# Optimization experiments

Measured on AMD Instinct MI355X. Metric: run time of the kernel, lower is better.

## Reference

```python
import jax, jax.numpy as jnp
import numpy as np

U = 256  # units


def _lstm_scan(x, W, R, bc):
    """Run the custom LSTM over time axis of x [B,T,D].

    W: (D,4U) stacked [ki|kf|ko|kc]; R: (U,4U) stacked [ri|rf|ro|rc]; bc: (U,).
    Faithful quirks: no bias on i/f/o gates; c_new = sigmoid(f*c + i*cand);
    h_new = tanh(c_new) * o.
    Returns (last_h [B,U], outputs [B,T,U]).
    """
    B = x.shape[0]
    xW = jnp.einsum('btd,dg->tbg', x, W)  # precompute input projections, (T,B,4U)

    def step(carry, xw):
        h, c = carry
        g = xw + h @ R  # (B,4U)
        i = jax.nn.sigmoid(g[:, 0 * U:1 * U])
        f = jax.nn.sigmoid(g[:, 1 * U:2 * U])
        o = jax.nn.sigmoid(g[:, 2 * U:3 * U])
        cand = jnp.tanh(g[:, 3 * U:4 * U] + bc)
        c_new = jax.nn.sigmoid(f * c + i * cand)
        h_new = jnp.tanh(c_new) * o
        return (h_new, c_new), h_new

    h0 = jnp.zeros((B, U), dtype=x.dtype)
    c0 = jnp.zeros((B, U), dtype=x.dtype)
    (h_last, _), hs = jax.lax.scan(step, (h0, c0), xW)
    return h_last, jnp.swapaxes(hs, 0, 1)  # (B,T,U)


def setup_inputs() -> dict:
    key = jax.random.key(0)
    ks = jax.random.split(key, 5)
    B, T, D = 16, 2048, 256
    s_in = 1.0 / np.sqrt(D)
    s_rec = 1.0 / np.sqrt(U)
    return {
        'x': jax.random.normal(ks[0], (B, T, D), dtype=jnp.float32),
        'W_f': jax.random.normal(ks[1], (D, 4 * U), dtype=jnp.float32) * s_in,
        'R_f': jax.random.normal(ks[2], (U, 4 * U), dtype=jnp.float32) * s_rec,
        'bc_f': jnp.zeros((U,), dtype=jnp.float32),
        'W_b': jax.random.normal(ks[3], (D, 4 * U), dtype=jnp.float32) * s_in,
        'R_b': jax.random.normal(ks[4], (U, 4 * U), dtype=jnp.float32) * s_rec,
        'bc_b': jnp.zeros((U,), dtype=jnp.float32),
    }


def reference(x, W_f, R_f, bc_f, W_b, R_b, bc_b):
    # forward direction
    _, out_f = _lstm_scan(x, W_f, R_f, bc_f)
    # backward direction: K.rnn(go_backwards=True) iterates reversed inputs and
    # returns outputs in iteration (reversed-time) order, NOT re-reversed.
    _, out_b = _lstm_scan(x[:, ::-1, :], W_b, R_b, bc_b)
    return jnp.concatenate([out_f, out_b], axis=-1)  # (B,T,2U)
```

## Files before the change

kernel.cpp:

```cpp
#include <hip/hip_runtime.h>
#include <hip/hip_bf16.h>
#include <hip/hip_fp16.h>

#define TT 2048
#define BB 16
#define DD 256
#define GG 1024
#define UU 256

using f32x4  = __attribute__((ext_vector_type(4))) float;
using short8 = __attribute__((ext_vector_type(8))) short;
using f16x8  = __attribute__((ext_vector_type(8))) _Float16;
using u32x4  = __attribute__((ext_vector_type(4))) unsigned int;

static __device__ __forceinline__ unsigned short f2h_u(float f){
  _Float16 h = (_Float16)f;
  return __builtin_bit_cast(unsigned short, h);
}
static __device__ __forceinline__ float h2f(unsigned short u){
  return (float)__builtin_bit_cast(_Float16, u);
}
static __device__ __forceinline__ unsigned short f2bf_u(float f){
  __hip_bfloat16 b = __float2bfloat16(f);
  return __builtin_bit_cast(unsigned short, b);
}
static __device__ __forceinline__ float sigmoid_f(float x){
  return 1.0f / (1.0f + __expf(-x));
}
static __device__ __forceinline__ float tanh_f(float x){
  float ax = fabsf(x);
  float e  = __expf(2.0f*ax);
  float r  = 1.0f - 2.0f/(e + 1.0f);
  return copysignf(r, x);
}
static __device__ __forceinline__ f32x4 mfma16x16x32_f16(f16x8 a, f16x8 b, f32x4 c){
  return __builtin_amdgcn_mfma_f32_16x16x32_f16(a, b, c, 0, 0, 0);
}
static __device__ __forceinline__ void lds_barrier(){
  __builtin_amdgcn_sched_barrier(0);
  asm volatile("s_waitcnt lgkmcnt(0)" ::: "memory");
  __builtin_amdgcn_s_barrier();
  __builtin_amdgcn_sched_barrier(0);
}

__global__ __launch_bounds__(256) void cvt_x_kernel(const float* __restrict__ x,
                                                    unsigned short* __restrict__ xh){
  int gid = blockIdx.x*256 + threadIdx.x;
  const float4* xv = (const float4*)x;
  float4 v = xv[gid];
  unsigned int u0 = (unsigned int)f2bf_u(v.x) | ((unsigned int)f2bf_u(v.y) << 16);
  unsigned int u1 = (unsigned int)f2bf_u(v.z) | ((unsigned int)f2bf_u(v.w) << 16);
  ((uint2*)xh)[gid] = make_uint2(u0, u1);
}

__global__ __launch_bounds__(256) void cvt_wt_kernel(const float* __restrict__ Wf,
                                                     const float* __restrict__ Wb,
                                                     unsigned short* __restrict__ wt){
  int gid = blockIdx.x*256 + threadIdx.x;
  int d   = gid >> 18;
  int rem = gid & 262143;
  int n   = rem >> 8;
  int k   = rem & 255;
  const float* src = d ? Wb : Wf;
  wt[gid] = f2bf_u(src[k*GG + n]);
}

__global__ __launch_bounds__(256) void cvt_rt_kernel(const float* __restrict__ Rf,
                                                     const float* __restrict__ Rb,
                                                     unsigned short* __restrict__ rt){
  int gid = blockIdx.x*256 + threadIdx.x;
  int d   = gid >> 18;
  int rem = gid & 262143;
  int c   = rem >> 8;
  int p   = rem & 255;
  int Qb  = c >> 7, tc = c & 127;
  int ul  = tc >> 2, g = tc & 3;
  int ucol = g*256 + Qb*32 + ul;
  int s = p >> 5, l4g = (p >> 3) & 3, e = p & 7;
  int k = 32*s + (e < 4 ? 4*l4g + e : 16 + 4*l4g + (e - 4));
  const float* src = d ? Rb : Rf;
  rt[gid] = f2h_u(src[k*GG + ucol]);
}

__global__ __launch_bounds__(256) void gemm_projT(const unsigned short* __restrict__ Ah,
                                                  const unsigned short* __restrict__ BTh,
                                                  unsigned short* __restrict__ Cd,
                                                  int xstart, int Tc){
  __shared__ __align__(16) unsigned short smem[18432];
  unsigned short* sA = smem;
  unsigned short* sB = smem + 9216;
  unsigned short* sC = smem;

  int mt  = blockIdx.x >> 3;
  int nt  = blockIdx.x & 7;
  int tid = threadIdx.x;

  const unsigned short* Bb = BTh + (size_t)nt*128*DD;

  int w = tid >> 6, lane = tid & 63, l15 = lane & 15, l4 = lane >> 4;
  int wm = w >> 1, wn = w & 1;

  f32x4 zero4 = {0.0f, 0.0f, 0.0f, 0.0f};
  f32x4 acc[4][4];
#pragma unroll
  for (int i = 0; i < 4; ++i)
#pragma unroll
    for (int j = 0; j < 4; ++j) acc[i][j] = zero4;

  for (int kt = 0; kt < 4; ++kt){
    __syncthreads();
#pragma unroll
    for (int i = 0; i < 4; ++i){
      int ch = tid + i*256;
      int r = ch >> 3, c8 = ch & 7;
      int bb = r >> 3, ti = r & 7;
      int tx = xstart + mt*8 + ti;
      *(uint4*)(sA + r*72 + c8*8) = *(const uint4*)(Ah + ((size_t)bb*TT + tx)*DD + kt*64 + c8*8);
      *(uint4*)(sB + r*72 + c8*8) = *(const uint4*)(Bb + (size_t)r*DD + kt*64 + c8*8);
    }
    __syncthreads();
#pragma unroll
    for (int ks = 0; ks < 2; ++ks){
      short8 a[4], b[4];
#pragma unroll
      for (int mf = 0; mf < 4; ++mf)
        a[mf] = *(const short8*)(sA + (wm*64 + mf*16 + l15)*72 + ks*32 + l4*8);
#pragma unroll
      for (int nf = 0; nf < 4; ++nf)
        b[nf] = *(const short8*)(sB + (wn*64 + nf*16 + l15)*72 + ks*32 + l4*8);
#pragma unroll
      for (int mf = 0; mf < 4; ++mf)
#pragma unroll
        for (int nf = 0; nf < 4; ++nf)
          acc[mf][nf] = __builtin_amdgcn_mfma_f32_16x16x32_bf16(a[mf], b[nf], acc[mf][nf], 0, 0, 0);
    }
  }
  __syncthreads();
#pragma unroll
  for (int mf = 0; mf < 4; ++mf)
#pragma unroll
    for (int nf = 0; nf < 4; ++nf)
#pragma unroll
      for (int r = 0; r < 4; ++r)
        sC[(wm*64 + mf*16 + l4*4 + r)*136 + wn*64 + nf*16 + l15] = f2h_u(acc[mf][nf][r]);
  __syncthreads();
  int c = tid >> 1, half = tid & 1;
#pragma unroll
  for (int ti = 0; ti < 8; ++ti){
    unsigned short* slab = Cd + ((size_t)(mt*8 + ti)*GG + nt*128)*16;
    unsigned short v[8];
#pragma unroll
    for (int j = 0; j < 8; ++j)
      v[j] = sC[((half*8 + j)*8 + ti)*136 + c];
    uint4 pk;
    pk.x = (unsigned int)v[0] | ((unsigned int)v[1] << 16);
    pk.y = (unsigned int)v[2] | ((unsigned int)v[3] << 16);
    pk.z = (unsigned int)v[4] | ((unsigned int)v[5] << 16);
    pk.w = (unsigned int)v[6] | ((unsigned int)v[7] << 16);
    *(uint4*)(slab + c*16 + half*8) = pk;
  }
}

template<int Q>
__device__ __forceinline__ void scan_body(
    unsigned short* hT,
    const unsigned short* __restrict__ projT,
    const unsigned short* __restrict__ rt,
    const float* __restrict__ bcf, const float* __restrict__ bcb,
    float* __restrict__ out,
    float* __restrict__ stH, float* __restrict__ stC,
    unsigned short* __restrict__ xchg,
    int* __restrict__ flags,
    int t0, int t1, int Tc, int first, int d)
{
  int tid = threadIdx.x;
  int w = tid >> 6, l = tid & 63, l15 = l & 15, l4 = l >> 4;

  u32x4 frag[8];
  {
    const unsigned short* Rd = rt + (size_t)d*262144
                             + ((size_t)(Q*128 + w*16 + l15))*256 + l4*8;
#pragma unroll
    for (int s = 0; s < 8; ++s)
      frag[s] = *(const u32x4*)(Rd + s*32);
  }
#pragma unroll
  for (int s = 0; s < 8; ++s)
    asm volatile("" : "+v"(frag[s]));

  const float* stHb = stH + d*4096;
  for (int idx = tid; idx < 4096; idx += 512){
    int b = idx >> 8, u = idx & 255;
    hT[(u >> 2)*68 + b*4 + (u & 3)] = first ? (unsigned short)0
                                            : f2h_u(stHb[b*256 + u]);
  }

  const int u_loc = 4*w + l4, u_g = 32*Q + u_loc;
  float c_r = 0.f, h_r = 0.f;
  if (!first) c_r = stC[(d*16 + l15)*256 + u_g];
  float bc_r = (d ? bcb : bcf)[u_g];

  const unsigned short* prj = projT + (size_t)d*Tc*16384;
  const int myflag = (d*8 + Q)*32;
  const int p = (Q + w) & 7;
  const int paflag = (d*8 + p)*32;
  const unsigned long long* xull = (const unsigned long long*)xchg;
  const int Tl = t1 - t0;

  __syncthreads();

  for (int s = 0; s < Tl; ++s){
    int t = t0 + s;
    int ps = d ? (Tl - 1 - s) : s;

    const unsigned short* pr = prj + (size_t)ps*16384;
    unsigned short pj0 = pr[(0*256 + u_g)*16 + l15];
    unsigned short pj1 = pr[(1*256 + u_g)*16 + l15];
    unsigned short pj2 = pr[(2*256 + u_g)*16 + l15];
    unsigned short pj3 = pr[(3*256 + u_g)*16 + l15];

    unsigned long long v0 = 0, v1 = 0;
    if (s > 0 && w >= 1){
      while (__hip_atomic_load(&flags[paflag], __ATOMIC_RELAXED, __HIP_MEMORY_SCOPE_AGENT) < s)
        __builtin_amdgcn_s_sleep(1);
      size_t base = (((size_t)d*2 + ((s - 1) & 1))*8 + p)*128;
      v0 = __hip_atomic_load(&xull[base + 2*l    ], __ATOMIC_RELAXED, __HIP_MEMORY_SCOPE_AGENT);
      v1 = __hip_atomic_load(&xull[base + 2*l + 1], __ATOMIC_RELAXED, __HIP_MEMORY_SCOPE_AGENT);
    }

    f32x4 acc = {0.f, 0.f, 0.f, 0.f};
    {
      uint2 b0 = *(const uint2*)&hT[(Q*8     + l4)*68 + l15*4];
      uint2 b1 = *(const uint2*)&hT[(Q*8 + 4 + l4)*68 + l15*4];
      u32x4 bv = {b0.x, b0.y, b1.x, b1.y};
      acc = mfma16x16x32_f16(__builtin_bit_cast(f16x8, frag[Q]),
                             __builtin_bit_cast(f16x8, bv), acc);
    }

    if (s > 0 && w >= 1){
      int uq = 8*p + (l >> 3), bq = 2*(l & 7);
      *(uint2*)&hT[uq*68 + bq*4    ] = make_uint2((unsigned)v0, (unsigned)(v0 >> 32));
      *(uint2*)&hT[uq*68 + bq*4 + 4] = make_uint2((unsigned)v1, (unsigned)(v1 >> 32));
    }
    lds_barrier();

#pragma unroll
    for (int j = 1; j < 8; ++j){
      const int sg = (Q + j) & 7;
      uint2 b0 = *(const uint2*)&hT[(sg*8     + l4)*68 + l15*4];
      uint2 b1 = *(const uint2*)&hT[(sg*8 + 4 + l4)*68 + l15*4];
      u32x4 bv = {b0.x, b0.y, b1.x, b1.y};
      acc = mfma16x16x32_f16(__builtin_bit_cast(f16x8, frag[sg]),
                             __builtin_bit_cast(f16x8, bv), acc);
    }

    float gi = acc[0] + h2f(pj0);
    float gf = acc[1] + h2f(pj1);
    float go = acc[2] + h2f(pj2);
    float gc = acc[3] + h2f(pj3) + bc_r;
    float ig = sigmoid_f(gi);
    float fg = sigmoid_f(gf);
    float og = sigmoid_f(go);
    float cand = tanh_f(gc);
    c_r = sigmoid_f(fg*c_r + ig*cand);
    float h = tanh_f(c_r) * og;
    h_r = h;

    unsigned short hu = f2h_u(h);
    hT[(8*Q + w)*68 + l15*4 + l4] = hu;
    xchg[((size_t)(d*2 + (s & 1))*8 + Q)*512 + w*64 + l15*4 + l4] = hu;
    __builtin_amdgcn_sched_barrier(0);
    out[((size_t)l15*TT + t)*512 + d*256 + u_g] = h;
    __builtin_amdgcn_sched_barrier(0);
    asm volatile("s_waitcnt vmcnt(1) lgkmcnt(0)" ::: "memory");
    __builtin_amdgcn_s_barrier();
    __builtin_amdgcn_sched_barrier(0);
    if (tid == 0)
      __hip_atomic_store(&flags[myflag], s + 1, __ATOMIC_RELAXED, __HIP_MEMORY_SCOPE_AGENT);
  }

  stC[(d*16 + l15)*256 + u_g] = c_r;
  stH[(d*16 + l15)*256 + u_g] = h_r;
}

__global__ __attribute__((amdgpu_flat_work_group_size(512, 512), amdgpu_waves_per_eu(2, 2)))
void lstm_scan_mfma(const unsigned short* __restrict__ projT,
                    const unsigned short* __restrict__ rt,
                    const float* __restrict__ bcf, const float* __restrict__ bcb,
                    float* __restrict__ out,
                    float* __restrict__ stH, float* __restrict__ stC,
                    unsigned short* __restrict__ xchg,
                    int* __restrict__ flags,
                    int t0, int t1, int Tc, int first)
{
  __shared__ __align__(16) unsigned short hT[64*68];
  int blk = blockIdx.x;
  int d = blk & 7, Q = blk >> 3;
  if (d >= 2) return;
  switch (Q){
    case 0: scan_body<0>(hT, projT, rt, bcf, bcb, out, stH, stC, xchg, flags, t0, t1, Tc, first, d); break;
    case 1: scan_body<1>(hT, projT, rt, bcf, bcb, out, stH, stC, xchg, flags, t0, t1, Tc, first, d); break;
    case 2: scan_body<2>(hT, projT, rt, bcf, bcb, out, stH, stC, xchg, flags, t0, t1, Tc, first, d); break;
    case 3: scan_body<3>(hT, projT, rt, bcf, bcb, out, stH, stC, xchg, flags, t0, t1, Tc, first, d); break;
    case 4: scan_body<4>(hT, projT, rt, bcf, bcb, out, stH, stC, xchg, flags, t0, t1, Tc, first, d); break;
    case 5: scan_body<5>(hT, projT, rt, bcf, bcb, out, stH, stC, xchg, flags, t0, t1, Tc, first, d); break;
    case 6: scan_body<6>(hT, projT, rt, bcf, bcb, out, stH, stC, xchg, flags, t0, t1, Tc, first, d); break;
    default: scan_body<7>(hT, projT, rt, bcf, bcb, out, stH, stC, xchg, flags, t0, t1, Tc, first, d); break;
  }
}

extern "C" void kernel_launch(void* const* d_in, const int* in_sizes, int n_in,
                              void* d_out, int out_size, void* d_ws, size_t ws_size,
                              hipStream_t stream){
  const float* x   = (const float*)d_in[0];
  const float* Wf  = (const float*)d_in[1];
  const float* Rf  = (const float*)d_in[2];
  const float* bcf = (const float*)d_in[3];
  const float* Wb  = (const float*)d_in[4];
  const float* Rb  = (const float*)d_in[5];
  const float* bcb = (const float*)d_in[6];
  float* out = (float*)d_out;
  char* ws = (char*)d_ws;

  const size_t OFF_XH    = 0;
  const size_t OFF_WT    = 16777216;
  const size_t OFF_RT    = OFF_WT + 1048576;
  const size_t OFF_STH   = OFF_RT + 1048576;
  const size_t OFF_STC   = OFF_STH + 32768;
  const size_t OFF_XCHG  = OFF_STC + 32768;
  const size_t OFF_FLAGS = OFF_XCHG + 32768;
  const size_t OFF_PROJT = OFF_FLAGS + 4096;

  unsigned short* xh    = (unsigned short*)(ws + OFF_XH);
  unsigned short* wt    = (unsigned short*)(ws + OFF_WT);
  unsigned short* rt    = (unsigned short*)(ws + OFF_RT);
  float*          stH   = (float*)(ws + OFF_STH);
  float*          stC   = (float*)(ws + OFF_STC);
  unsigned short* xchg  = (unsigned short*)(ws + OFF_XCHG);
  int*            flags = (int*)(ws + OFF_FLAGS);
  unsigned short* projT = (unsigned short*)(ws + OFF_PROJT);

  int Tc = TT;
  while (Tc > 128 && OFF_PROJT + (size_t)65536*Tc > ws_size) Tc >>= 1;

  cvt_x_kernel<<<8192, 256, 0, stream>>>(x, xh);
  cvt_wt_kernel<<<2048, 256, 0, stream>>>(Wf, Wb, wt);
  cvt_rt_kernel<<<2048, 256, 0, stream>>>(Rf, Rb, rt);

  int nch = TT / Tc;
  for (int ch = 0; ch < nch; ++ch){
    int t0 = ch*Tc, t1 = t0 + Tc;
    gemm_projT<<<Tc, 256, 0, stream>>>(xh, wt,          projT,                     t0,      Tc);
    gemm_projT<<<Tc, 256, 0, stream>>>(xh, wt + 262144, projT + (size_t)Tc*GG*16,  TT - t1, Tc);
    hipMemsetAsync(flags, 0, 2048, stream);
    lstm_scan_mfma<<<64, 512, 0, stream>>>(projT, rt, bcf, bcb, out, stH, stC, xchg, flags,
                                           t0, t1, Tc, ch == 0 ? 1 : 0);
  }
}
```

Before: 3.460 ms.

## Feed MFMA B operands directly from exchange buffer, drop mid-step LDS barrier

Each wave now polls all seven peer flags with a wave-wide any(), then loads the peers' h slices straight from the global exchange buffer into registers as MFMA B fragments. Its own block's slice is read from a double-buffered 512-element LDS slab. This removes the LDS scatter of peer data and the barrier that sat between the first MFMA and the remaining seven, and the R layout permutation is simplified to match the new slab layout. In exchange, every wave now waits on all peers and issues seven times more global loads per step, so the polling and L2 traffic may grow.

```diff
diff --git a/kernel.cpp b/kernel.cpp
--- a/kernel.cpp
+++ b/kernel.cpp
@@ -36,11 +36,8 @@
 static __device__ __forceinline__ f32x4 mfma16x16x32_f16(f16x8 a, f16x8 b, f32x4 c){
   return __builtin_amdgcn_mfma_f32_16x16x32_f16(a, b, c, 0, 0, 0);
 }
-static __device__ __forceinline__ void lds_barrier(){
-  __builtin_amdgcn_sched_barrier(0);
-  asm volatile("s_waitcnt lgkmcnt(0)" ::: "memory");
-  __builtin_amdgcn_s_barrier();
-  __builtin_amdgcn_sched_barrier(0);
+static __device__ __forceinline__ unsigned int pk2(float a, float b){
+  return (unsigned int)f2h_u(a) | ((unsigned int)f2h_u(b) << 16);
 }
 
 __global__ __launch_bounds__(256) void cvt_x_kernel(const float* __restrict__ x,
@@ -76,10 +73,8 @@
   int Qb  = c >> 7, tc = c & 127;
   int ul  = tc >> 2, g = tc & 3;
   int ucol = g*256 + Qb*32 + ul;
-  int s = p >> 5, l4g = (p >> 3) & 3, e = p & 7;
-  int k = 32*s + (e < 4 ? 4*l4g + e : 16 + 4*l4g + (e - 4));
   const float* src = d ? Rb : Rf;
-  rt[gid] = f2h_u(src[k*GG + ucol]);
+  rt[gid] = f2h_u(src[p*GG + ucol]);
 }
 
 __global__ __launch_bounds__(256) void gemm_projT(const unsigned short* __restrict__ Ah,
@@ -163,7 +158,7 @@
 
 template<int Q>
 __device__ __forceinline__ void scan_body(
-    unsigned short* hT,
+    unsigned short (*hT)[512],
     const unsigned short* __restrict__ projT,
     const unsigned short* __restrict__ rt,
     const float* __restrict__ bcf, const float* __restrict__ bcb,
@@ -188,22 +183,19 @@
   for (int s = 0; s < 8; ++s)
     asm volatile("" : "+v"(frag[s]));
 
-  const float* stHb = stH + d*4096;
-  for (int idx = tid; idx < 4096; idx += 512){
-    int b = idx >> 8, u = idx & 255;
-    hT[(u >> 2)*68 + b*4 + (u & 3)] = first ? (unsigned short)0
-                                            : f2h_u(stHb[b*256 + u]);
-  }
-
-  const int u_loc = 4*w + l4, u_g = 32*Q + u_loc;
+  const int ul = 4*w + l4;
+  const int u_g = 32*Q + ul;
+  const int uq4 = ul >> 3, ue = ul & 7;
+  const int slabpos = uq4*128 + l15*8 + ue;
+
   float c_r = 0.f, h_r = 0.f;
   if (!first) c_r = stC[(d*16 + l15)*256 + u_g];
   float bc_r = (d ? bcb : bcf)[u_g];
 
   const unsigned short* prj = projT + (size_t)d*Tc*16384;
   const int myflag = (d*8 + Q)*32;
-  const int p = (Q + w) & 7;
-  const int paflag = (d*8 + p)*32;
+  const int pl = (Q + 1 + (l < 7 ? l : 0)) & 7;
+  const int* pfaddr = &flags[(d*8 + pl)*32];
   const unsigned long long* xull = (const unsigned long long*)xchg;
   const int Tl = t1 - t0;
 
@@ -219,39 +211,46 @@
     unsigned short pj2 = pr[(2*256 + u_g)*16 + l15];
     unsigned short pj3 = pr[(3*256 + u_g)*16 + l15];
 
-    unsigned long long v0 = 0, v1 = 0;
-    if (s > 0 && w >= 1){
-      while (__hip_atomic_load(&flags[paflag], __ATOMIC_RELAXED, __HIP_MEMORY_SCOPE_AGENT) < s)
+    u32x4 fb[8];
+    if (s == 0){
+      if (first){
+#pragma unroll
+        for (int p = 0; p < 8; ++p) fb[p] = (u32x4){0u, 0u, 0u, 0u};
+      } else {
+#pragma unroll
+        for (int p = 0; p < 8; ++p){
+          const float* hb = stH + (size_t)(d*16 + l15)*256 + 32*p + 8*l4;
+          float4 a = *(const float4*)hb;
+          float4 b = *(const float4*)(hb + 4);
+          fb[p] = (u32x4){pk2(a.x, a.y), pk2(a.z, a.w), pk2(b.x, b.y), pk2(b.z, b.w)};
+        }
+      }
+    } else {
+      for (;;){
+        int v = __hip_atomic_load(pfaddr, __ATOMIC_RELAXED, __HIP_MEMORY_SCOPE_AGENT);
+        if (!__any(l < 7 && v < s)) break;
         __builtin_amdgcn_s_sleep(1);
-      size_t base = (((size_t)d*2 + ((s - 1) & 1))*8 + p)*128;
-      v0 = __hip_atomic_load(&xull[base + 2*l    ], __ATOMIC_RELAXED, __HIP_MEMORY_SCOPE_AGENT);
-      v1 = __hip_atomic_load(&xull[base + 2*l + 1], __ATOMIC_RELAXED, __HIP_MEMORY_SCOPE_AGENT);
+      }
+      asm volatile("" ::: "memory");
+      size_t sb = ((size_t)d*2 + ((s - 1) & 1))*8;
+#pragma unroll
+      for (int j = 1; j < 8; ++j){
+        const int p = (Q + j) & 7;
+        size_t base = (sb + p)*128 + l4*32 + l15*2;
+        unsigned long long v0 = __hip_atomic_load(&xull[base    ], __ATOMIC_RELAXED, __HIP_MEMORY_SCOPE_AGENT);
+        unsigned long long v1 = __hip_atomic_load(&xull[base + 1], __ATOMIC_RELAXED, __HIP_MEMORY_SCOPE_AGENT);
+        fb[p] = (u32x4){(unsigned)v0, (unsigned)(v0 >> 32),
+                        (unsigned)v1, (unsigned)(v1 >> 32)};
+      }
+      fb[Q] = *(const u32x4*)&hT[s & 1][l4*128 + l15*8];
     }
 
     f32x4 acc = {0.f, 0.f, 0.f, 0.f};
-    {
-      uint2 b0 = *(const uint2*)&hT[(Q*8     + l4)*68 + l15*4];
-      uint2 b1 = *(const uint2*)&hT[(Q*8 + 4 + l4)*68 + l15*4];
-      u32x4 bv = {b0.x, b0.y, b1.x, b1.y};
-      acc = mfma16x16x32_f16(__builtin_bit_cast(f16x8, frag[Q]),
-                             __builtin_bit_cast(f16x8, bv), acc);
-    }
-
-    if (s > 0 && w >= 1){
-      int uq = 8*p + (l >> 3), bq = 2*(l & 7);
-      *(uint2*)&hT[uq*68 + bq*4    ] = make_uint2((unsigned)v0, (unsigned)(v0 >> 32));
-      *(uint2*)&hT[uq*68 + bq*4 + 4] = make_uint2((unsigned)v1, (unsigned)(v1 >> 32));
-    }
-    lds_barrier();
-
-#pragma unroll
-    for (int j = 1; j < 8; ++j){
+#pragma unroll
+    for (int j = 0; j < 8; ++j){
       const int sg = (Q + j) & 7;
-      uint2 b0 = *(const uint2*)&hT[(sg*8     + l4)*68 + l15*4];
-      uint2 b1 = *(const uint2*)&hT[(sg*8 + 4 + l4)*68 + l15*4];
-      u32x4 bv = {b0.x, b0.y, b1.x, b1.y};
       acc = mfma16x16x32_f16(__builtin_bit_cast(f16x8, frag[sg]),
-                             __builtin_bit_cast(f16x8, bv), acc);
+                             __builtin_bit_cast(f16x8, fb[sg]), acc);
     }
 
     float gi = acc[0] + h2f(pj0);
@@ -267,8 +266,8 @@
     h_r = h;
 
     unsigned short hu = f2h_u(h);
-    hT[(8*Q + w)*68 + l15*4 + l4] = hu;
-    xchg[((size_t)(d*2 + (s & 1))*8 + Q)*512 + w*64 + l15*4 + l4] = hu;
+    hT[(s + 1) & 1][slabpos] = hu;
+    xchg[((size_t)(d*2 + (s & 1))*8 + Q)*512 + slabpos] = hu;
     __builtin_amdgcn_sched_barrier(0);
     out[((size_t)l15*TT + t)*512 + d*256 + u_g] = h;
     __builtin_amdgcn_sched_barrier(0);
@@ -293,7 +292,7 @@
                     int* __restrict__ flags,
                     int t0, int t1, int Tc, int first)
 {
-  __shared__ __align__(16) unsigned short hT[64*68];
+  __shared__ __align__(16) unsigned short hT[2][512];
   int blk = blockIdx.x;
   int d = blk & 7, Q = blk >> 3;
   if (d >= 2) return;
```

Result: slower. 4.274 ms (+23.5%).
